# Performance work log

Measured on AMD Instinct MI355X. Metric: run time of the kernel, lower is better.

The kernel has to match this reference:

```python
import jax, jax.numpy as jnp
import numpy as np

V, D = 100000, 128
B, C, K = 16384, 10, 20

def setup_inputs() -> dict:
    key = jax.random.key(0)
    k1, k2, k3, k4, k5 = jax.random.split(key, 5)
    return {
        "context": jax.random.randint(k1, (B, C), 0, V),
        "target": jax.random.randint(k2, (B,), 0, V),
        "negative_samples": jax.random.randint(k3, (B, K), 0, V),
        "emb_W": jax.random.normal(k4, (V, D), dtype=jnp.float32),
        "ctx_W": jax.random.normal(k5, (V, D), dtype=jnp.float32),
    }

def reference(context, target, negative_samples, emb_W, ctx_W):
    target_emb = emb_W[target]                      # [B, D]
    context_emb = ctx_W[context].mean(axis=1)       # [B, C, D] -> [B, D]
    neg_emb = ctx_W[negative_samples]               # [B, K, D]
    pos_score = jax.nn.log_sigmoid(jnp.sum(context_emb * target_emb, axis=1))  # [B]
    neg_logits = jnp.einsum("bkd,bd->bk", neg_emb, context_emb)               # [B, K]
    neg_score = jax.nn.log_sigmoid(-neg_logits).sum(axis=1)                   # [B]
    return -(pos_score + neg_score).mean()
```

## Files before the change

kernel.cpp:

```cpp
#include <hip/hip_runtime.h>

#define BB 16384
#define CC 10
#define KK 20
#define DD 128

__device__ __forceinline__ float lsg(float x) {
    return fminf(x, 0.0f) - __logf(1.0f + __expf(-fabsf(x)));
}

template <int MASK>
__device__ __forceinline__ float swz_add(float v) {
    int r = __builtin_amdgcn_ds_swizzle(__float_as_int(v), MASK);
    return v + __int_as_float(r);
}

__device__ __forceinline__ float dot4(float4 a, float4 b) {
    return a.x * b.x + a.y * b.y + a.z * b.z + a.w * b.w;
}

__global__ __launch_bounds__(256) void w2v_loss_kernel(
    const int*   __restrict__ context,
    const int*   __restrict__ target,
    const int*   __restrict__ negs,
    const float* __restrict__ embW,
    const float* __restrict__ ctxW,
    float*       __restrict__ block_part
) {
    const int wave  = threadIdx.x >> 6;
    const int lane  = threadIdx.x & 63;
    const int group = lane >> 4;
    const int gl    = lane & 15;

    const int b = blockIdx.x * 16 + wave * 4 + group;

    const float4* ctxW4 = reinterpret_cast<const float4*>(ctxW);
    const float4* embW4 = reinterpret_cast<const float4*>(embW);

    const int* cbase = context + b * CC;
    const int* nbase = negs    + b * KK;

    float4 accA = make_float4(0.f, 0.f, 0.f, 0.f);
    float4 accB = make_float4(0.f, 0.f, 0.f, 0.f);
    #pragma unroll
    for (int c = 0; c < CC; ++c) {
        const size_t row = (size_t)cbase[c] * (DD / 4);
        const float4 vA = ctxW4[row + gl];
        const float4 vB = ctxW4[row + 16 + gl];
        accA.x += vA.x; accA.y += vA.y; accA.z += vA.z; accA.w += vA.w;
        accB.x += vB.x; accB.y += vB.y; accB.z += vB.z; accB.w += vB.w;
    }
    const float inv = 1.0f / CC;
    accA.x *= inv; accA.y *= inv; accA.z *= inv; accA.w *= inv;
    accB.x *= inv; accB.y *= inv; accB.z *= inv; accB.w *= inv;

    const size_t trow = (size_t)target[b] * (DD / 4);
    float pd = dot4(accA, embW4[trow + gl]) + dot4(accB, embW4[trow + 16 + gl]);

    float nd[KK];
    #pragma unroll
    for (int k = 0; k < KK; ++k) {
        const size_t row = (size_t)nbase[k] * (DD / 4);
        nd[k] = dot4(accA, ctxW4[row + gl]) + dot4(accB, ctxW4[row + 16 + gl]);
    }

    pd = swz_add<0x041F>(pd);
    #pragma unroll
    for (int k = 0; k < KK; ++k) nd[k] = swz_add<0x041F>(nd[k]);
    pd = swz_add<0x081F>(pd);
    #pragma unroll
    for (int k = 0; k < KK; ++k) nd[k] = swz_add<0x081F>(nd[k]);
    pd = swz_add<0x101F>(pd);
    #pragma unroll
    for (int k = 0; k < KK; ++k) nd[k] = swz_add<0x101F>(nd[k]);
    pd = swz_add<0x201F>(pd);
    #pragma unroll
    for (int k = 0; k < KK; ++k) nd[k] = swz_add<0x201F>(nd[k]);

    float score = lsg(pd);
    #pragma unroll
    for (int k = 0; k < KK; ++k) score += lsg(-nd[k]);

    float s = swz_add<0x401F>(score);
    s += __shfl_xor(s, 32, 64);

    __shared__ float sp[4];
    if (lane == 0) sp[wave] = s;
    __syncthreads();
    if (threadIdx.x == 0)
        block_part[blockIdx.x] = sp[0] + sp[1] + sp[2] + sp[3];
}

__global__ __launch_bounds__(256) void w2v_finish_kernel(
    const float* __restrict__ part, float* __restrict__ out, int n, float scale)
{
    __shared__ float sm[4];
    float s = 0.f;
    for (int i = threadIdx.x; i < n; i += 256) s += part[i];
    #pragma unroll
    for (int off = 32; off; off >>= 1) s += __shfl_xor(s, off, 64);
    const int wave = threadIdx.x >> 6;
    const int lane = threadIdx.x & 63;
    if (lane == 0) sm[wave] = s;
    __syncthreads();
    if (threadIdx.x == 0) out[0] = (sm[0] + sm[1] + sm[2] + sm[3]) * scale;
}

extern "C" void kernel_launch(void* const* d_in, const int* in_sizes, int n_in,
                              void* d_out, int out_size, void* d_ws, size_t ws_size,
                              hipStream_t stream) {
    const int*   context = (const int*)d_in[0];
    const int*   target  = (const int*)d_in[1];
    const int*   negs    = (const int*)d_in[2];
    const float* embW    = (const float*)d_in[3];
    const float* ctxW    = (const float*)d_in[4];
    float* out = (float*)d_out;

    float* block_part = (float*)d_ws;
    const int nblocks = BB / 16;

    w2v_loss_kernel<<<nblocks, 256, 0, stream>>>(context, target, negs, embW, ctxW, block_part);
    w2v_finish_kernel<<<1, 256, 0, stream>>>(block_part, out, nblocks, -1.0f / (float)BB);
}
```

Before: 43.50 us.

## Assign 32 lanes per sample with one float4 each, batch negative-row loads

Result: slower. 47.25 us (+8.6%).

```diff
diff --git a/kernel.cpp b/kernel.cpp
--- a/kernel.cpp
+++ b/kernel.cpp
@@ -19,7 +19,7 @@
     return a.x * b.x + a.y * b.y + a.z * b.z + a.w * b.w;
 }
 
-__global__ __launch_bounds__(256) void w2v_loss_kernel(
+__global__ __launch_bounds__(256, 8) void w2v_loss_kernel(
     const int*   __restrict__ context,
     const int*   __restrict__ target,
     const int*   __restrict__ negs,
@@ -29,10 +29,10 @@
 ) {
     const int wave  = threadIdx.x >> 6;
     const int lane  = threadIdx.x & 63;
-    const int group = lane >> 4;
-    const int gl    = lane & 15;
+    const int group = lane >> 5;
+    const int gl    = lane & 31;
 
-    const int b = blockIdx.x * 16 + wave * 4 + group;
+    const int b = blockIdx.x * 8 + wave * 2 + group;
 
     const float4* ctxW4 = reinterpret_cast<const float4*>(ctxW);
     const float4* embW4 = reinterpret_cast<const float4*>(embW);
@@ -40,28 +40,35 @@
     const int* cbase = context + b * CC;
     const int* nbase = negs    + b * KK;
 
-    float4 accA = make_float4(0.f, 0.f, 0.f, 0.f);
-    float4 accB = make_float4(0.f, 0.f, 0.f, 0.f);
+    int cidx[CC];
+    #pragma unroll
+    for (int c = 0; c < CC; ++c) cidx[c] = cbase[c];
+    const int tidx = target[b];
+
+    float4 acc = make_float4(0.f, 0.f, 0.f, 0.f);
     #pragma unroll
     for (int c = 0; c < CC; ++c) {
-        const size_t row = (size_t)cbase[c] * (DD / 4);
-        const float4 vA = ctxW4[row + gl];
-        const float4 vB = ctxW4[row + 16 + gl];
-        accA.x += vA.x; accA.y += vA.y; accA.z += vA.z; accA.w += vA.w;
-        accB.x += vB.x; accB.y += vB.y; accB.z += vB.z; accB.w += vB.w;
+        const float4 v = ctxW4[(size_t)cidx[c] * (DD / 4) + gl];
+        acc.x += v.x; acc.y += v.y; acc.z += v.z; acc.w += v.w;
     }
     const float inv = 1.0f / CC;
-    accA.x *= inv; accA.y *= inv; accA.z *= inv; accA.w *= inv;
-    accB.x *= inv; accB.y *= inv; accB.z *= inv; accB.w *= inv;
+    acc.x *= inv; acc.y *= inv; acc.z *= inv; acc.w *= inv;
 
-    const size_t trow = (size_t)target[b] * (DD / 4);
-    float pd = dot4(accA, embW4[trow + gl]) + dot4(accB, embW4[trow + 16 + gl]);
+    float pd = dot4(acc, embW4[(size_t)tidx * (DD / 4) + gl]);
 
     float nd[KK];
     #pragma unroll
-    for (int k = 0; k < KK; ++k) {
-        const size_t row = (size_t)nbase[k] * (DD / 4);
-        nd[k] = dot4(accA, ctxW4[row + gl]) + dot4(accB, ctxW4[row + 16 + gl]);
+    for (int k = 0; k < KK; k += 4) {
+        const int i0 = nbase[k + 0], i1 = nbase[k + 1];
+        const int i2 = nbase[k + 2], i3 = nbase[k + 3];
+        const float4 v0 = ctxW4[(size_t)i0 * (DD / 4) + gl];
+        const float4 v1 = ctxW4[(size_t)i1 * (DD / 4) + gl];
+        const float4 v2 = ctxW4[(size_t)i2 * (DD / 4) + gl];
+        const float4 v3 = ctxW4[(size_t)i3 * (DD / 4) + gl];
+        nd[k + 0] = dot4(acc, v0);
+        nd[k + 1] = dot4(acc, v1);
+        nd[k + 2] = dot4(acc, v2);
+        nd[k + 3] = dot4(acc, v3);
     }
 
     pd = swz_add<0x041F>(pd);
@@ -76,13 +83,15 @@
     pd = swz_add<0x201F>(pd);
     #pragma unroll
     for (int k = 0; k < KK; ++k) nd[k] = swz_add<0x201F>(nd[k]);
+    pd = swz_add<0x401F>(pd);
+    #pragma unroll
+    for (int k = 0; k < KK; ++k) nd[k] = swz_add<0x401F>(nd[k]);
 
     float score = lsg(pd);
     #pragma unroll
     for (int k = 0; k < KK; ++k) score += lsg(-nd[k]);
 
-    float s = swz_add<0x401F>(score);
-    s += __shfl_xor(s, 32, 64);
+    float s = score + __shfl_xor(score, 32, 64);
 
     __shared__ float sp[4];
     if (lane == 0) sp[wave] = s;
@@ -117,7 +126,7 @@
     float* out = (float*)d_out;
 
     float* block_part = (float*)d_ws;
-    const int nblocks = BB / 16;
+    const int nblocks = BB / 8;
 
     w2v_loss_kernel<<<nblocks, 256, 0, stream>>>(context, target, negs, embW, ctxW, block_part);
     w2v_finish_kernel<<<1, 256, 0, stream>>>(block_part, out, nblocks, -1.0f / (float)BB);
```
